# Kernel optimization log

Hardware: AMD Instinct MI355X
Metric: run time of the kernel (lower is better)

## Reference

```python
import jax, jax.numpy as jnp
import numpy as np

N_NODES = 50000
N_EDGES = 800000
IN_CH = 128
HID_CH = 128


def glorot(key, shape):
    fan_in, fan_out = shape[0], shape[1]
    lim = np.sqrt(6.0 / (fan_in + fan_out)).astype(np.float32)
    return jax.random.uniform(key, shape, jnp.float32, -lim, lim)


def setup_inputs() -> dict:
    key = jax.random.key(0)
    k1, k2, k3, k4 = jax.random.split(key, 4)
    x = jax.random.normal(k1, (N_NODES, IN_CH), jnp.float32)
    edge_index = jax.random.randint(k2, (2, N_EDGES), 0, N_NODES, jnp.int64)
    W1 = glorot(k3, (IN_CH, HID_CH))
    b1 = jnp.zeros((HID_CH,), jnp.float32)
    W2 = glorot(k4, (HID_CH, HID_CH))
    b2 = jnp.zeros((HID_CH,), jnp.float32)
    return {"x": x, "edge_index": edge_index, "W1": W1, "b1": b1, "W2": W2, "b2": b2}


def _gcn_conv(x, W, b, src, dst, n_nodes):
    # PyG GCNConv: h = D^{-1/2} (A + I) D^{-1/2} (x W) + b
    h = x @ W  # [N, H] transform first (as in PyG)
    loops = jnp.arange(n_nodes, dtype=src.dtype)
    s = jnp.concatenate([src, loops])  # add self-loops
    d = jnp.concatenate([dst, loops])
    deg = jnp.zeros((n_nodes,), h.dtype).at[d].add(1.0)
    dinv = jnp.where(deg > 0, jax.lax.rsqrt(deg), 0.0)
    coef = dinv[s] * dinv[d]  # [E+N]
    msg = h[s] * coef[:, None]  # gather + scale
    out = jax.ops.segment_sum(msg, d, num_segments=n_nodes)  # scatter-add
    return out + b


def reference(x, edge_index, W1, b1, W2, b2):
    src, dst = edge_index[0], edge_index[1]
    n = x.shape[0]
    h = jax.nn.relu(_gcn_conv(x, W1, b1, src, dst, n))
    h = jax.nn.relu(_gcn_conv(h, W2, b2, src, dst, n))
    return h
```

## Files before the change

### kernel.cpp

```cpp
#include <hip/hip_runtime.h>

#define N_NODES 50000
#define N_EDGES 800000
#define CH 128
#define NBUCK 196
#define B_BIN 250
#define CHUNK 3200

typedef __attribute__((ext_vector_type(8))) short bf16x8;
typedef __attribute__((ext_vector_type(4))) float f32x4;

__device__ __forceinline__ float bf2f(unsigned short u) {
    union { unsigned int i; float f; } c;
    c.i = ((unsigned int)u) << 16;
    return c.f;
}
__device__ __forceinline__ unsigned short f2bf(float f) {
    union { float f; unsigned int i; } c;
    c.f = f;
    unsigned int lsb = (c.i >> 16) & 1u;
    c.i += 0x7fffu + lsb;
    return (unsigned short)(c.i >> 16);
}

__global__ __launch_bounds__(256) void k_bin_count(const int* __restrict__ dst,
                                                   int* __restrict__ blk_base) {
    __shared__ int h[NBUCK];
    const int tid = threadIdx.x, b = blockIdx.x;
    for (int i = tid; i < NBUCK; i += 256) h[i] = 0;
    __syncthreads();
    const int e0 = b * CHUNK;
    for (int i = tid; i < CHUNK; i += 256)
        atomicAdd(&h[dst[e0 + i] >> 8], 1);
    __syncthreads();
    for (int k = tid; k < NBUCK; k += 256)
        blk_base[b * NBUCK + k] = h[k];
}

__global__ __launch_bounds__(256) void k_colscan(int* __restrict__ blk_base,
                                                 int* __restrict__ bucket_cnt) {
    __shared__ int sm[256];
    const int tid = threadIdx.x, k = blockIdx.x;
    int v = (tid < B_BIN) ? blk_base[tid * NBUCK + k] : 0;
    sm[tid] = v;
    __syncthreads();
    #pragma unroll
    for (int off = 1; off < 256; off <<= 1) {
        int t = (tid >= off) ? sm[tid - off] : 0;
        __syncthreads();
        sm[tid] += t;
        __syncthreads();
    }
    if (tid < B_BIN) blk_base[tid * NBUCK + k] = sm[tid] - v;
    if (tid == 255) bucket_cnt[k] = sm[255];
}

__global__ __launch_bounds__(256) void k_scan_buckets(const int* __restrict__ bucket_cnt,
                                                      int* __restrict__ bucket_base) {
    __shared__ int sm[256];
    const int tid = threadIdx.x;
    int v = (tid < NBUCK) ? bucket_cnt[tid] : 0;
    sm[tid] = v;
    __syncthreads();
    #pragma unroll
    for (int off = 1; off < 256; off <<= 1) {
        int t = (tid >= off) ? sm[tid - off] : 0;
        __syncthreads();
        sm[tid] += t;
        __syncthreads();
    }
    if (tid < NBUCK) bucket_base[tid] = sm[tid] - v;
    if (tid == 0) bucket_base[NBUCK] = N_EDGES;
}

__global__ __launch_bounds__(256) void k_bin_place(const int* __restrict__ ei,
                                                   const int* __restrict__ bucket_base,
                                                   const int* __restrict__ blk_base,
                                                   unsigned int* __restrict__ ebuf) {
    __shared__ int h[NBUCK];
    const int tid = threadIdx.x, b = blockIdx.x;
    for (int i = tid; i < NBUCK; i += 256) h[i] = 0;
    __syncthreads();
    const int e0 = b * CHUNK;
    for (int i = tid; i < CHUNK; i += 256) {
        int s = ei[e0 + i];
        int d = ei[N_EDGES + e0 + i];
        int k = d >> 8;
        int loc = atomicAdd(&h[k], 1);
        int pos = bucket_base[k] + blk_base[b * NBUCK + k] + loc;
        ebuf[pos] = ((unsigned int)s << 8) | (unsigned int)(d & 255);
    }
}

__global__ __launch_bounds__(256) void k_bucket_csr(const unsigned int* __restrict__ ebuf,
                                                    const int* __restrict__ bucket_base,
                                                    int* __restrict__ rowptr,
                                                    int* __restrict__ col,
                                                    float* __restrict__ dinv) {
    __shared__ int cnts[256];
    __shared__ int fillc[256];
    __shared__ int sm[256];
    const int tid = threadIdx.x, k = blockIdx.x;
    const int node0 = k << 8;
    const int e0 = bucket_base[k], e1 = bucket_base[k + 1];
    const int cnt = e1 - e0;

    cnts[tid] = 0;
    __syncthreads();
    for (int i = tid; i < cnt; i += 256)
        atomicAdd(&cnts[ebuf[e0 + i] & 255], 1);
    __syncthreads();

    int v = cnts[tid];
    sm[tid] = v;
    __syncthreads();
    #pragma unroll
    for (int off = 1; off < 256; off <<= 1) {
        int t = (tid >= off) ? sm[tid - off] : 0;
        __syncthreads();
        sm[tid] += t;
        __syncthreads();
    }
    int rp = sm[tid] - v;
    fillc[tid] = rp;
    int node = node0 + tid;
    if (node < N_NODES) {
        rowptr[node] = e0 + rp;
        dinv[node] = rsqrtf((float)(v + 1));
    }
    if (k == NBUCK - 1 && tid == 0) rowptr[N_NODES] = N_EDGES;
    __syncthreads();

    for (int i = tid; i < cnt; i += 256) {
        unsigned int pv = ebuf[e0 + i];
        int j = pv & 255;
        int loc = atomicAdd(&fillc[j], 1);
        col[e0 + loc] = (int)(pv >> 8);
    }
}

__global__ __launch_bounds__(256) void k_wt(const float* __restrict__ Wa,
                                            const float* __restrict__ Wb,
                                            unsigned short* __restrict__ Wta,
                                            unsigned short* __restrict__ Wtb) {
    const float* W = blockIdx.x ? Wb : Wa;
    unsigned short* Wt = blockIdx.x ? Wtb : Wta;
    const int tid = threadIdx.x;
    for (int i = 0; i < 64; ++i) {
        int idx = i * 256 + tid;
        int n = idx >> 7, kk = idx & 127;
        Wt[idx] = f2bf(W[kk * CH + n]);
    }
}

__global__ __launch_bounds__(256) void k_xb(const float* __restrict__ X,
                                            unsigned short* __restrict__ XB) {
    int t = blockIdx.x * 256 + threadIdx.x;
    int base = t * 8;
    float4 a = *(const float4*)&X[base];
    float4 b = *(const float4*)&X[base + 4];
    ushort4 lo, hi;
    lo.x = f2bf(a.x); lo.y = f2bf(a.y); lo.z = f2bf(a.z); lo.w = f2bf(a.w);
    hi.x = f2bf(b.x); hi.y = f2bf(b.y); hi.z = f2bf(b.z); hi.w = f2bf(b.w);
    *(ushort4*)&XB[base] = lo;
    *(ushort4*)&XB[base + 4] = hi;
}

__global__ __launch_bounds__(256) void k_gemm_mfma(
        const unsigned short* __restrict__ A,
        const unsigned short* __restrict__ Wt,
        const float* __restrict__ dinv,
        unsigned short* __restrict__ HS) {
    const int tid = threadIdx.x;
    const int l = tid & 63, w = tid >> 6;
    const int lm = l & 15, lk = l >> 4;
    const int row0 = blockIdx.x * 64 + w * 16;

    int arow = row0 + lm;
    if (arow >= N_NODES) arow = N_NODES - 1;
    bf16x8 a[4];
    #pragma unroll
    for (int ki = 0; ki < 4; ++ki)
        a[ki] = *(const bf16x8*)&A[arow * CH + ki * 32 + lk * 8];

    float dv[4];
    int rowr[4];
    #pragma unroll
    for (int r = 0; r < 4; ++r) {
        rowr[r] = row0 + lk * 4 + r;
        dv[r] = dinv[rowr[r] < N_NODES ? rowr[r] : 0];
    }

    #pragma unroll
    for (int ct = 0; ct < 8; ++ct) {
        const unsigned short* wp = &Wt[(ct * 16 + lm) * CH + lk * 8];
        f32x4 acc = {0.f, 0.f, 0.f, 0.f};
        #pragma unroll
        for (int ki = 0; ki < 4; ++ki) {
            bf16x8 bfrag = *(const bf16x8*)&wp[ki * 32];
            acc = __builtin_amdgcn_mfma_f32_16x16x32_bf16(a[ki], bfrag, acc, 0, 0, 0);
        }
        #pragma unroll
        for (int r = 0; r < 4; ++r) {
            if (rowr[r] < N_NODES)
                HS[rowr[r] * CH + ct * 16 + lm] = f2bf(acc[r] * dv[r]);
        }
    }
}

template <int MODE>
__global__ __launch_bounds__(256) void k_aggregate(
        const int* __restrict__ rowptr, const int* __restrict__ col,
        const unsigned short* __restrict__ HS, const float* __restrict__ dinv,
        const float* __restrict__ b, float* __restrict__ OUTF,
        unsigned short* __restrict__ OUTB) {
    int gid = blockIdx.x * 256 + threadIdx.x;
    int node = gid >> 5;
    if (node >= N_NODES) return;
    int lane = gid & 31;
    const ushort4* H4 = (const ushort4*)HS;

    int e0 = rowptr[node];
    int e1 = rowptr[node + 1];

    ushort4 hself = H4[node * 32 + lane];
    float ax = bf2f(hself.x), ay = bf2f(hself.y), az = bf2f(hself.z), aw = bf2f(hself.w);

    int e = e0;
    for (; e + 3 < e1; e += 4) {
        int s0 = col[e], s1 = col[e + 1], s2 = col[e + 2], s3 = col[e + 3];
        ushort4 v0 = H4[s0 * 32 + lane];
        ushort4 v1 = H4[s1 * 32 + lane];
        ushort4 v2 = H4[s2 * 32 + lane];
        ushort4 v3 = H4[s3 * 32 + lane];
        ax += (bf2f(v0.x) + bf2f(v1.x)) + (bf2f(v2.x) + bf2f(v3.x));
        ay += (bf2f(v0.y) + bf2f(v1.y)) + (bf2f(v2.y) + bf2f(v3.y));
        az += (bf2f(v0.z) + bf2f(v1.z)) + (bf2f(v2.z) + bf2f(v3.z));
        aw += (bf2f(v0.w) + bf2f(v1.w)) + (bf2f(v2.w) + bf2f(v3.w));
    }
    for (; e < e1; ++e) {
        ushort4 va = H4[col[e] * 32 + lane];
        ax += bf2f(va.x); ay += bf2f(va.y); az += bf2f(va.z); aw += bf2f(va.w);
    }

    float di = dinv[node];
    float4 bb = *(const float4*)&b[lane * 4];
    float ox = fmaxf(ax * di + bb.x, 0.f);
    float oy = fmaxf(ay * di + bb.y, 0.f);
    float oz = fmaxf(az * di + bb.z, 0.f);
    float ow = fmaxf(aw * di + bb.w, 0.f);
    if (MODE == 0) {
        ushort4 o;
        o.x = f2bf(ox); o.y = f2bf(oy); o.z = f2bf(oz); o.w = f2bf(ow);
        *(ushort4*)&OUTB[node * CH + lane * 4] = o;
    } else {
        *(float4*)&OUTF[node * CH + lane * 4] = make_float4(ox, oy, oz, ow);
    }
}

extern "C" void kernel_launch(void* const* d_in, const int* in_sizes, int n_in,
                              void* d_out, int out_size, void* d_ws, size_t ws_size,
                              hipStream_t stream) {
    const float* x  = (const float*)d_in[0];
    const int*   ei = (const int*)d_in[1];
    const float* W1 = (const float*)d_in[2];
    const float* b1 = (const float*)d_in[3];
    const float* W2 = (const float*)d_in[4];
    const float* b2 = (const float*)d_in[5];
    float* out = (float*)d_out;

    int* blk_base    = (int*)d_ws;
    int* bucket_cnt  = blk_base + 49152;
    int* bucket_base = bucket_cnt + 256;
    int* rowptr      = bucket_base + 256;
    int* col         = rowptr + 50176;
    float* dinv      = (float*)(col + 800256);
    unsigned int* ebuf = (unsigned int*)(dinv + 50176);
    unsigned short* xb  = (unsigned short*)(ebuf + 800256);
    unsigned short* hb  = xb + 6400000;
    unsigned short* hs  = hb + 6400000;
    unsigned short* wt1 = hs + 6400000;
    unsigned short* wt2 = wt1 + 16384;

    const int gG = (N_NODES + 63) / 64;
    const int gA = (N_NODES * 32 + 255) / 256;
    const int gX = 3125;

    k_bin_count<<<B_BIN, 256, 0, stream>>>(ei + N_EDGES, blk_base);
    k_colscan<<<NBUCK, 256, 0, stream>>>(blk_base, bucket_cnt);
    k_scan_buckets<<<1, 256, 0, stream>>>(bucket_cnt, bucket_base);
    k_bin_place<<<B_BIN, 256, 0, stream>>>(ei, bucket_base, blk_base, ebuf);
    k_bucket_csr<<<NBUCK, 256, 0, stream>>>(ebuf, bucket_base, rowptr, col, dinv);

    k_wt<<<2, 256, 0, stream>>>(W1, W2, wt1, wt2);
    k_xb<<<gX, 256, 0, stream>>>(x, xb);

    k_gemm_mfma<<<gG, 256, 0, stream>>>(xb, wt1, dinv, hs);
    k_aggregate<0><<<gA, 256, 0, stream>>>(rowptr, col, hs, dinv, b1, nullptr, hb);

    k_gemm_mfma<<<gG, 256, 0, stream>>>(hb, wt2, dinv, hs);
    k_aggregate<1><<<gA, 256, 0, stream>>>(rowptr, col, hs, dinv, b2, out, nullptr);
}
```

Before: 160.4 us.

## Fuse GCN pipeline: overlap binning with GEMM1, fuse aggregate with GEMM2

The first GEMM now reads fp32 x directly and converts it to bf16 in registers. It runs in the same launch as the edge-binning count blocks and no longer scales by dinv, so it does not have to wait for the degree computation. The bucket scan is folded into the placement and CSR kernels, and the layer-1 aggregation is fused with the layer-2 GEMM through shared memory. Together these remove several launches and the xb and hb round-trips. In exchange, layer-1 aggregation now gathers dinv per edge, which adds scattered reads, and both the placement and CSR kernels redundantly rerun the bucket scan in every block.

Result: no change. 161.0 us (+0.4%).

```diff
diff --git a/kernel.cpp b/kernel.cpp
--- a/kernel.cpp
+++ b/kernel.cpp
@@ -6,6 +6,7 @@
 #define NBUCK 196
 #define B_BIN 250
 #define CHUNK 3200
+#define G_GEMM 782
 
 typedef __attribute__((ext_vector_type(8))) short bf16x8;
 typedef __attribute__((ext_vector_type(4))) float f32x4;
@@ -21,122 +22,6 @@
     unsigned int lsb = (c.i >> 16) & 1u;
     c.i += 0x7fffu + lsb;
     return (unsigned short)(c.i >> 16);
-}
-
-__global__ __launch_bounds__(256) void k_bin_count(const int* __restrict__ dst,
-                                                   int* __restrict__ blk_base) {
-    __shared__ int h[NBUCK];
-    const int tid = threadIdx.x, b = blockIdx.x;
-    for (int i = tid; i < NBUCK; i += 256) h[i] = 0;
-    __syncthreads();
-    const int e0 = b * CHUNK;
-    for (int i = tid; i < CHUNK; i += 256)
-        atomicAdd(&h[dst[e0 + i] >> 8], 1);
-    __syncthreads();
-    for (int k = tid; k < NBUCK; k += 256)
-        blk_base[b * NBUCK + k] = h[k];
-}
-
-__global__ __launch_bounds__(256) void k_colscan(int* __restrict__ blk_base,
-                                                 int* __restrict__ bucket_cnt) {
-    __shared__ int sm[256];
-    const int tid = threadIdx.x, k = blockIdx.x;
-    int v = (tid < B_BIN) ? blk_base[tid * NBUCK + k] : 0;
-    sm[tid] = v;
-    __syncthreads();
-    #pragma unroll
-    for (int off = 1; off < 256; off <<= 1) {
-        int t = (tid >= off) ? sm[tid - off] : 0;
-        __syncthreads();
-        sm[tid] += t;
-        __syncthreads();
-    }
-    if (tid < B_BIN) blk_base[tid * NBUCK + k] = sm[tid] - v;
-    if (tid == 255) bucket_cnt[k] = sm[255];
-}
-
-__global__ __launch_bounds__(256) void k_scan_buckets(const int* __restrict__ bucket_cnt,
-                                                      int* __restrict__ bucket_base) {
-    __shared__ int sm[256];
-    const int tid = threadIdx.x;
-    int v = (tid < NBUCK) ? bucket_cnt[tid] : 0;
-    sm[tid] = v;
-    __syncthreads();
-    #pragma unroll
-    for (int off = 1; off < 256; off <<= 1) {
-        int t = (tid >= off) ? sm[tid - off] : 0;
-        __syncthreads();
-        sm[tid] += t;
-        __syncthreads();
-    }
-    if (tid < NBUCK) bucket_base[tid] = sm[tid] - v;
-    if (tid == 0) bucket_base[NBUCK] = N_EDGES;
-}
-
-__global__ __launch_bounds__(256) void k_bin_place(const int* __restrict__ ei,
-                                                   const int* __restrict__ bucket_base,
-                                                   const int* __restrict__ blk_base,
-                                                   unsigned int* __restrict__ ebuf) {
-    __shared__ int h[NBUCK];
-    const int tid = threadIdx.x, b = blockIdx.x;
-    for (int i = tid; i < NBUCK; i += 256) h[i] = 0;
-    __syncthreads();
-    const int e0 = b * CHUNK;
-    for (int i = tid; i < CHUNK; i += 256) {
-        int s = ei[e0 + i];
-        int d = ei[N_EDGES + e0 + i];
-        int k = d >> 8;
-        int loc = atomicAdd(&h[k], 1);
-        int pos = bucket_base[k] + blk_base[b * NBUCK + k] + loc;
-        ebuf[pos] = ((unsigned int)s << 8) | (unsigned int)(d & 255);
-    }
-}
-
-__global__ __launch_bounds__(256) void k_bucket_csr(const unsigned int* __restrict__ ebuf,
-                                                    const int* __restrict__ bucket_base,
-                                                    int* __restrict__ rowptr,
-                                                    int* __restrict__ col,
-                                                    float* __restrict__ dinv) {
-    __shared__ int cnts[256];
-    __shared__ int fillc[256];
-    __shared__ int sm[256];
-    const int tid = threadIdx.x, k = blockIdx.x;
-    const int node0 = k << 8;
-    const int e0 = bucket_base[k], e1 = bucket_base[k + 1];
-    const int cnt = e1 - e0;
-
-    cnts[tid] = 0;
-    __syncthreads();
-    for (int i = tid; i < cnt; i += 256)
-        atomicAdd(&cnts[ebuf[e0 + i] & 255], 1);
-    __syncthreads();
-
-    int v = cnts[tid];
-    sm[tid] = v;
-    __syncthreads();
-    #pragma unroll
-    for (int off = 1; off < 256; off <<= 1) {
-        int t = (tid >= off) ? sm[tid - off] : 0;
-        __syncthreads();
-        sm[tid] += t;
-        __syncthreads();
-    }
-    int rp = sm[tid] - v;
-    fillc[tid] = rp;
-    int node = node0 + tid;
-    if (node < N_NODES) {
-        rowptr[node] = e0 + rp;
-        dinv[node] = rsqrtf((float)(v + 1));
-    }
-    if (k == NBUCK - 1 && tid == 0) rowptr[N_NODES] = N_EDGES;
-    __syncthreads();
-
-    for (int i = tid; i < cnt; i += 256) {
-        unsigned int pv = ebuf[e0 + i];
-        int j = pv & 255;
-        int loc = atomicAdd(&fillc[j], 1);
-        col[e0 + loc] = (int)(pv >> 8);
-    }
 }
 
 __global__ __launch_bounds__(256) void k_wt(const float* __restrict__ Wa,
@@ -153,47 +38,51 @@
     }
 }
 
-__global__ __launch_bounds__(256) void k_xb(const float* __restrict__ X,
-                                            unsigned short* __restrict__ XB) {
-    int t = blockIdx.x * 256 + threadIdx.x;
-    int base = t * 8;
-    float4 a = *(const float4*)&X[base];
-    float4 b = *(const float4*)&X[base + 4];
-    ushort4 lo, hi;
-    lo.x = f2bf(a.x); lo.y = f2bf(a.y); lo.z = f2bf(a.z); lo.w = f2bf(a.w);
-    hi.x = f2bf(b.x); hi.y = f2bf(b.y); hi.z = f2bf(b.z); hi.w = f2bf(b.w);
-    *(ushort4*)&XB[base] = lo;
-    *(ushort4*)&XB[base + 4] = hi;
-}
-
-__global__ __launch_bounds__(256) void k_gemm_mfma(
-        const unsigned short* __restrict__ A,
-        const unsigned short* __restrict__ Wt,
-        const float* __restrict__ dinv,
-        unsigned short* __restrict__ HS) {
+__global__ __launch_bounds__(256) void k_mega(
+        const int* __restrict__ ei, int* __restrict__ blk_base,
+        const float* __restrict__ X, const unsigned short* __restrict__ Wt1,
+        unsigned short* __restrict__ HS1u) {
     const int tid = threadIdx.x;
+    const int b = blockIdx.x;
+
+    if (b < B_BIN) {
+        __shared__ int h[NBUCK];
+        for (int i = tid; i < NBUCK; i += 256) h[i] = 0;
+        __syncthreads();
+        const int e0 = b * CHUNK;
+        const int* dst = ei + N_EDGES;
+        for (int i = tid; i < CHUNK; i += 256)
+            atomicAdd(&h[dst[e0 + i] >> 8], 1);
+        __syncthreads();
+        for (int k = tid; k < NBUCK; k += 256)
+            blk_base[b * NBUCK + k] = h[k];
+        return;
+    }
+
+    const int gb = b - B_BIN;
     const int l = tid & 63, w = tid >> 6;
     const int lm = l & 15, lk = l >> 4;
-    const int row0 = blockIdx.x * 64 + w * 16;
+    const int row0 = gb * 64 + w * 16;
 
     int arow = row0 + lm;
     if (arow >= N_NODES) arow = N_NODES - 1;
     bf16x8 a[4];
     #pragma unroll
-    for (int ki = 0; ki < 4; ++ki)
-        a[ki] = *(const bf16x8*)&A[arow * CH + ki * 32 + lk * 8];
-
-    float dv[4];
-    int rowr[4];
-    #pragma unroll
-    for (int r = 0; r < 4; ++r) {
-        rowr[r] = row0 + lk * 4 + r;
-        dv[r] = dinv[rowr[r] < N_NODES ? rowr[r] : 0];
+    for (int ki = 0; ki < 4; ++ki) {
+        const float* ap = &X[arow * CH + ki * 32 + lk * 8];
+        float4 f0 = *(const float4*)ap;
+        float4 f1 = *(const float4*)(ap + 4);
+        bf16x8 af;
+        af[0] = (short)f2bf(f0.x); af[1] = (short)f2bf(f0.y);
+        af[2] = (short)f2bf(f0.z); af[3] = (short)f2bf(f0.w);
+        af[4] = (short)f2bf(f1.x); af[5] = (short)f2bf(f1.y);
+        af[6] = (short)f2bf(f1.z); af[7] = (short)f2bf(f1.w);
+        a[ki] = af;
     }
 
     #pragma unroll
     for (int ct = 0; ct < 8; ++ct) {
-        const unsigned short* wp = &Wt[(ct * 16 + lm) * CH + lk * 8];
+        const unsigned short* wp = &Wt1[(ct * 16 + lm) * CH + lk * 8];
         f32x4 acc = {0.f, 0.f, 0.f, 0.f};
         #pragma unroll
         for (int ki = 0; ki < 4; ++ki) {
@@ -202,18 +91,213 @@
         }
         #pragma unroll
         for (int r = 0; r < 4; ++r) {
-            if (rowr[r] < N_NODES)
-                HS[rowr[r] * CH + ct * 16 + lm] = f2bf(acc[r] * dv[r]);
-        }
-    }
-}
-
-template <int MODE>
-__global__ __launch_bounds__(256) void k_aggregate(
+            int row = row0 + lk * 4 + r;
+            if (row < N_NODES)
+                HS1u[row * CH + ct * 16 + lm] = f2bf(acc[r]);
+        }
+    }
+}
+
+__global__ __launch_bounds__(256) void k_colscan(int* __restrict__ blk_base,
+                                                 int* __restrict__ bucket_cnt) {
+    __shared__ int sm[256];
+    const int tid = threadIdx.x, k = blockIdx.x;
+    int v = (tid < B_BIN) ? blk_base[tid * NBUCK + k] : 0;
+    sm[tid] = v;
+    __syncthreads();
+    #pragma unroll
+    for (int off = 1; off < 256; off <<= 1) {
+        int t = (tid >= off) ? sm[tid - off] : 0;
+        __syncthreads();
+        sm[tid] += t;
+        __syncthreads();
+    }
+    if (tid < B_BIN) blk_base[tid * NBUCK + k] = sm[tid] - v;
+    if (tid == 255) bucket_cnt[k] = sm[255];
+}
+
+__global__ __launch_bounds__(256) void k_bin_place(const int* __restrict__ ei,
+                                                   const int* __restrict__ bucket_cnt,
+                                                   const int* __restrict__ blk_base,
+                                                   unsigned int* __restrict__ ebuf) {
+    __shared__ int sm[256];
+    __shared__ int bbase[NBUCK];
+    __shared__ int h[NBUCK];
+    const int tid = threadIdx.x, b = blockIdx.x;
+
+    int v = (tid < NBUCK) ? bucket_cnt[tid] : 0;
+    sm[tid] = v;
+    __syncthreads();
+    #pragma unroll
+    for (int off = 1; off < 256; off <<= 1) {
+        int t = (tid >= off) ? sm[tid - off] : 0;
+        __syncthreads();
+        sm[tid] += t;
+        __syncthreads();
+    }
+    if (tid < NBUCK) bbase[tid] = sm[tid] - v;
+    for (int i = tid; i < NBUCK; i += 256) h[i] = 0;
+    __syncthreads();
+
+    const int e0 = b * CHUNK;
+    for (int i = tid; i < CHUNK; i += 256) {
+        int s = ei[e0 + i];
+        int d = ei[N_EDGES + e0 + i];
+        int k = d >> 8;
+        int loc = atomicAdd(&h[k], 1);
+        int pos = bbase[k] + blk_base[b * NBUCK + k] + loc;
+        ebuf[pos] = ((unsigned int)s << 8) | (unsigned int)(d & 255);
+    }
+}
+
+__global__ __launch_bounds__(256) void k_bucket_csr(const unsigned int* __restrict__ ebuf,
+                                                    const int* __restrict__ bucket_cnt,
+                                                    int* __restrict__ rowptr,
+                                                    int* __restrict__ col,
+                                                    float* __restrict__ dinv) {
+    __shared__ int cnts[256];
+    __shared__ int fillc[256];
+    __shared__ int sm[256];
+    __shared__ int e0s;
+    const int tid = threadIdx.x, k = blockIdx.x;
+    const int node0 = k << 8;
+
+    int vb = (tid < NBUCK) ? bucket_cnt[tid] : 0;
+    sm[tid] = vb;
+    __syncthreads();
+    #pragma unroll
+    for (int off = 1; off < 256; off <<= 1) {
+        int t = (tid >= off) ? sm[tid - off] : 0;
+        __syncthreads();
+        sm[tid] += t;
+        __syncthreads();
+    }
+    if (tid == k) e0s = sm[tid] - vb;
+    cnts[tid] = 0;
+    __syncthreads();
+    const int e0 = e0s;
+    const int cnt = bucket_cnt[k];
+
+    for (int i = tid; i < cnt; i += 256)
+        atomicAdd(&cnts[ebuf[e0 + i] & 255], 1);
+    __syncthreads();
+
+    int v = cnts[tid];
+    sm[tid] = v;
+    __syncthreads();
+    #pragma unroll
+    for (int off = 1; off < 256; off <<= 1) {
+        int t = (tid >= off) ? sm[tid - off] : 0;
+        __syncthreads();
+        sm[tid] += t;
+        __syncthreads();
+    }
+    int rp = sm[tid] - v;
+    fillc[tid] = rp;
+    int node = node0 + tid;
+    if (node < N_NODES) {
+        rowptr[node] = e0 + rp;
+        dinv[node] = rsqrtf((float)(v + 1));
+    }
+    if (k == NBUCK - 1 && tid == 0) rowptr[N_NODES] = N_EDGES;
+    __syncthreads();
+
+    for (int i = tid; i < cnt; i += 256) {
+        unsigned int pv = ebuf[e0 + i];
+        int j = pv & 255;
+        int loc = atomicAdd(&fillc[j], 1);
+        col[e0 + loc] = (int)(pv >> 8);
+    }
+}
+
+__global__ __launch_bounds__(256) void k_agg_gemm(
+        const int* __restrict__ rowptr, const int* __restrict__ col,
+        const unsigned short* __restrict__ HS1u, const float* __restrict__ dinv,
+        const float* __restrict__ b1, const unsigned short* __restrict__ Wt2,
+        unsigned short* __restrict__ HS2) {
+    __shared__ __align__(16) unsigned short hl[64 * 136];
+    const int tid = threadIdx.x;
+    const int node0 = blockIdx.x * 64;
+    const int lane = tid & 31;
+    const ushort4* H4 = (const ushort4*)HS1u;
+
+    float4 bb = *(const float4*)&b1[lane * 4];
+
+    #pragma unroll 2
+    for (int pass = 0; pass < 8; ++pass) {
+        int nl = pass * 8 + (tid >> 5);
+        int node = node0 + nl;
+        if (node < N_NODES) {
+            int e0 = rowptr[node];
+            int e1 = rowptr[node + 1];
+            float dd = dinv[node];
+
+            ushort4 hv = H4[node * 32 + lane];
+            float ax = bf2f(hv.x) * dd, ay = bf2f(hv.y) * dd;
+            float az = bf2f(hv.z) * dd, aw = bf2f(hv.w) * dd;
+
+            int e = e0;
+            for (; e + 3 < e1; e += 4) {
+                int s0 = col[e], s1 = col[e + 1], s2 = col[e + 2], s3 = col[e + 3];
+                float d0 = dinv[s0], d1 = dinv[s1], d2 = dinv[s2], d3 = dinv[s3];
+                ushort4 v0 = H4[s0 * 32 + lane];
+                ushort4 v1 = H4[s1 * 32 + lane];
+                ushort4 v2 = H4[s2 * 32 + lane];
+                ushort4 v3 = H4[s3 * 32 + lane];
+                ax += bf2f(v0.x) * d0 + bf2f(v1.x) * d1 + bf2f(v2.x) * d2 + bf2f(v3.x) * d3;
+                ay += bf2f(v0.y) * d0 + bf2f(v1.y) * d1 + bf2f(v2.y) * d2 + bf2f(v3.y) * d3;
+                az += bf2f(v0.z) * d0 + bf2f(v1.z) * d1 + bf2f(v2.z) * d2 + bf2f(v3.z) * d3;
+                aw += bf2f(v0.w) * d0 + bf2f(v1.w) * d1 + bf2f(v2.w) * d2 + bf2f(v3.w) * d3;
+            }
+            for (; e < e1; ++e) {
+                int s = col[e];
+                float ds = dinv[s];
+                ushort4 va = H4[s * 32 + lane];
+                ax += bf2f(va.x) * ds; ay += bf2f(va.y) * ds;
+                az += bf2f(va.z) * ds; aw += bf2f(va.w) * ds;
+            }
+
+            ushort4 o;
+            o.x = f2bf(fmaxf(ax * dd + bb.x, 0.f));
+            o.y = f2bf(fmaxf(ay * dd + bb.y, 0.f));
+            o.z = f2bf(fmaxf(az * dd + bb.z, 0.f));
+            o.w = f2bf(fmaxf(aw * dd + bb.w, 0.f));
+            *(ushort4*)&hl[nl * 136 + lane * 4] = o;
+        }
+    }
+    __syncthreads();
+
+    const int l = tid & 63, w = tid >> 6;
+    const int lm = l & 15, lk = l >> 4;
+    const int row0 = node0 + w * 16;
+
+    bf16x8 a[4];
+    #pragma unroll
+    for (int ki = 0; ki < 4; ++ki)
+        a[ki] = *(const bf16x8*)&hl[(w * 16 + lm) * 136 + ki * 32 + lk * 8];
+
+    #pragma unroll
+    for (int ct = 0; ct < 8; ++ct) {
+        const unsigned short* wp = &Wt2[(ct * 16 + lm) * CH + lk * 8];
+        f32x4 acc = {0.f, 0.f, 0.f, 0.f};
+        #pragma unroll
+        for (int ki = 0; ki < 4; ++ki) {
+            bf16x8 bfrag = *(const bf16x8*)&wp[ki * 32];
+            acc = __builtin_amdgcn_mfma_f32_16x16x32_bf16(a[ki], bfrag, acc, 0, 0, 0);
+        }
+        #pragma unroll
+        for (int r = 0; r < 4; ++r) {
+            int row = row0 + lk * 4 + r;
+            if (row < N_NODES)
+                HS2[row * CH + ct * 16 + lm] = f2bf(acc[r] * dinv[row]);
+        }
+    }
+}
+
+__global__ __launch_bounds__(256) void k_agg_final(
         const int* __restrict__ rowptr, const int* __restrict__ col,
         const unsigned short* __restrict__ HS, const float* __restrict__ dinv,
-        const float* __restrict__ b, float* __restrict__ OUTF,
-        unsigned short* __restrict__ OUTB) {
+        const float* __restrict__ b, float* __restrict__ OUT) {
     int gid = blockIdx.x * 256 + threadIdx.x;
     int node = gid >> 5;
     if (node >= N_NODES) return;
@@ -245,17 +329,12 @@
 
     float di = dinv[node];
     float4 bb = *(const float4*)&b[lane * 4];
-    float ox = fmaxf(ax * di + bb.x, 0.f);
-    float oy = fmaxf(ay * di + bb.y, 0.f);
-    float oz = fmaxf(az * di + bb.z, 0.f);
-    float ow = fmaxf(aw * di + bb.w, 0.f);
-    if (MODE == 0) {
-        ushort4 o;
-        o.x = f2bf(ox); o.y = f2bf(oy); o.z = f2bf(oz); o.w = f2bf(ow);
-        *(ushort4*)&OUTB[node * CH + lane * 4] = o;
-    } else {
-        *(float4*)&OUTF[node * CH + lane * 4] = make_float4(ox, oy, oz, ow);
-    }
+    float4 o;
+    o.x = fmaxf(ax * di + bb.x, 0.f);
+    o.y = fmaxf(ay * di + bb.y, 0.f);
+    o.z = fmaxf(az * di + bb.z, 0.f);
+    o.w = fmaxf(aw * di + bb.w, 0.f);
+    *(float4*)&OUT[node * CH + lane * 4] = o;
 }
 
 extern "C" void kernel_launch(void* const* d_in, const int* in_sizes, int n_in,
@@ -271,33 +350,22 @@
 
     int* blk_base    = (int*)d_ws;
     int* bucket_cnt  = blk_base + 49152;
-    int* bucket_base = bucket_cnt + 256;
-    int* rowptr      = bucket_base + 256;
+    int* rowptr      = bucket_cnt + 256;
     int* col         = rowptr + 50176;
     float* dinv      = (float*)(col + 800256);
     unsigned int* ebuf = (unsigned int*)(dinv + 50176);
-    unsigned short* xb  = (unsigned short*)(ebuf + 800256);
-    unsigned short* hb  = xb + 6400000;
-    unsigned short* hs  = hb + 6400000;
-    unsigned short* wt1 = hs + 6400000;
-    unsigned short* wt2 = wt1 + 16384;
-
-    const int gG = (N_NODES + 63) / 64;
+    unsigned short* hs1u = (unsigned short*)(ebuf + 800256);
+    unsigned short* hs2  = hs1u + 6400000;
+    unsigned short* wt1  = hs2 + 6400000;
+    unsigned short* wt2  = wt1 + 16384;
+
     const int gA = (N_NODES * 32 + 255) / 256;
-    const int gX = 3125;
-
-    k_bin_count<<<B_BIN, 256, 0, stream>>>(ei + N_EDGES, blk_base);
+
+    k_wt<<<2, 256, 0, stream>>>(W1, W2, wt1, wt2);
+    k_mega<<<B_BIN + G_GEMM, 256, 0, stream>>>(ei, blk_base, x, wt1, hs1u);
     k_colscan<<<NBUCK, 256, 0, stream>>>(blk_base, bucket_cnt);
-    k_scan_buckets<<<1, 256, 0, stream>>>(bucket_cnt, bucket_base);
-    k_bin_place<<<B_BIN, 256, 0, stream>>>(ei, bucket_base, blk_base, ebuf);
-    k_bucket_csr<<<NBUCK, 256, 0, stream>>>(ebuf, bucket_base, rowptr, col, dinv);
-
-    k_wt<<<2, 256, 0, stream>>>(W1, W2, wt1, wt2);
-    k_xb<<<gX, 256, 0, stream>>>(x, xb);
-
-    k_gemm_mfma<<<gG, 256, 0, stream>>>(xb, wt1, dinv, hs);
-    k_aggregate<0><<<gA, 256, 0, stream>>>(rowptr, col, hs, dinv, b1, nullptr, hb);
-
-    k_gemm_mfma<<<gG, 256, 0, stream>>>(hb, wt2, dinv, hs);
-    k_aggregate<1><<<gA, 256, 0, stream>>>(rowptr, col, hs, dinv, b2, out, nullptr);
-}
+    k_bin_place<<<B_BIN, 256, 0, stream>>>(ei, bucket_cnt, blk_base, ebuf);
+    k_bucket_csr<<<NBUCK, 256, 0, stream>>>(ebuf, bucket_cnt, rowptr, col, dinv);
+    k_agg_gemm<<<G_GEMM, 256, 0, stream>>>(rowptr, col, hs1u, dinv, b1, wt2, hs2);
+    k_agg_final<<<gA, 256, 0, stream>>>(rowptr, col, hs2, dinv, b2, out);
+}
```
